# Kernel optimization log

Hardware: AMD Instinct MI355X
Metric: run time of the kernel (lower is better)

Reference implementation:

```python
import jax, jax.numpy as jnp
import numpy as np


def _scattering(image, mags, phases):
    # image: [B,S,S] real; mags/phases: [J,L,S,S] real (Fourier-domain Morlet filters)
    J = mags.shape[0]
    psi = (mags * jnp.exp(1j * phases)).astype(jnp.complex64)        # [J,L,S,S]
    xf = jnp.fft.fft2(image)                                          # [B,S,S] complex64
    # first-order: modulus of wavelet convolutions, all scales/orientations at once
    u1 = jnp.abs(jnp.fft.ifft2(xf[:, None, None] * psi[None]))        # [B,J,L,S,S]
    s0 = image.mean(axis=(-2, -1))                                    # [B]
    s1 = u1.mean(axis=(2, 3, 4))                                      # [B,J] (orientation-averaged)
    # second-order: only j2 > j1 (the nan-filtered entries in the original)
    s2_parts = []
    for j1 in range(J - 1):  # structural loop over scales, not data dims
        u1f = jnp.fft.fft2(u1[:, j1].astype(jnp.complex64))           # [B,L1,S,S]
        psi2 = psi[j1 + 1:]                                           # [J2,L2,S,S]
        v = jnp.abs(jnp.fft.ifft2(u1f[:, :, None, None] * psi2[None, None]))  # [B,L1,J2,L2,S,S]
        s2_parts.append(v.mean(axis=(1, 3, 4, 5)))                    # [B,J2]
    s2 = jnp.concatenate(s2_parts, axis=1)                            # [B, J*(J-1)/2]
    return s0, s1, s2


def setup_inputs() -> dict:
    key = jax.random.key(0)
    ks = jax.random.split(key, 8)
    B, S, J, L = 64, 128, 6, 4
    return {
        "image_batch": jax.random.normal(ks[0], (B, S, S), dtype=jnp.float32),
        "mags": jax.random.uniform(ks[1], (J, L, S, S), dtype=jnp.float32),
        "phases": jax.random.normal(ks[2], (J, L, S, S), dtype=jnp.float32),
        "w1": jax.random.normal(ks[3], (22, 16), dtype=jnp.float32) * 0.1,
        "b1": jnp.zeros((16,), dtype=jnp.float32),
        "w2": jax.random.normal(ks[4], (16, 16), dtype=jnp.float32) * 0.1,
        "b2": jnp.zeros((16,), dtype=jnp.float32),
        "w3": jax.random.normal(ks[5], (16, 1), dtype=jnp.float32) * 0.1,
        "b3": jnp.zeros((1,), dtype=jnp.float32),
    }


def reference(image_batch, mags, phases, w1, b1, w2, b2, w3, b3):
    s0, s1, s2 = _scattering(image_batch, mags, phases)
    x = jnp.concatenate([s0[:, None], s1, s2], axis=1)                # [B,22]
    x = jax.nn.relu(x @ w1 + b1)
    x = jax.nn.relu(x @ w2 + b2)
    x = jax.nn.sigmoid(x @ w3 + b3)
    return jnp.squeeze(x, axis=1)                                     # [B]
```

## Files before the change

kernel.cpp:

```cpp
#include <hip/hip_runtime.h>
#include <math.h>


#define SDIM 128
#define PLANE 16384
#define PITCH 129
#define NT 1024
#define TWO_PI 6.28318530717958647692f
#define PSIH_SCALE 16.0f
#define A_SCALE 16.0f

typedef _Float16 h2 __attribute__((ext_vector_type(2)));

constexpr float W16R[8] = {1.f, 0.9238795325f, 0.7071067812f, 0.3826834324f,
                           0.f, -0.3826834324f, -0.7071067812f, -0.9238795325f};
constexpr float W16I[8] = {0.f, -0.3826834324f, -0.7071067812f, -0.9238795325f,
                           -1.f, -0.9238795325f, -0.7071067812f, -0.3826834324f};

__device__ __forceinline__ float fast_sqrtf(float x) { return __builtin_amdgcn_sqrtf(x); }

__device__ __forceinline__ unsigned packbf(float re, float im) {
  const unsigned r = __float_as_uint(re) + 0x8000u;
  const unsigned i = __float_as_uint(im) + 0x8000u;
  return __builtin_amdgcn_perm(r, i, 0x07060302u);
}
__device__ __forceinline__ void unpackbf(unsigned u, float& re, float& im) {
  re = __uint_as_float(u & 0xFFFF0000u);
  im = __uint_as_float(u << 16);
}

union UHU { unsigned u; h2 h; };
__device__ __forceinline__ h2 u2h(unsigned u) { UHU x; x.u = u; return x.h; }
__device__ __forceinline__ unsigned h2u(h2 h) { UHU x; x.h = h; return x.u; }
__device__ __forceinline__ h2 bch2(float f) { const _Float16 h = (_Float16)f; h2 v = {h, h}; return v; }
__device__ __forceinline__ h2 mkh2(float a, float b) { h2 v = {(_Float16)a, (_Float16)b}; return v; }

#define SEL_LO 0x05040100u
#define SEL_HI 0x07060302u

__device__ __forceinline__ void stC(float2* s, int idx, float re, float im) { s[idx] = make_float2(re, im); }
__device__ __forceinline__ void ldC(const float2* s, int idx, float& re, float& im) { const float2 v = s[idx]; re = v.x; im = v.y; }
__device__ __forceinline__ void stC(unsigned* s, int idx, float re, float im) { s[idx] = packbf(re, im); }
__device__ __forceinline__ void ldC(const unsigned* s, int idx, float& re, float& im) { unpackbf(s[idx], re, im); }

__device__ __forceinline__ void load_tw(const float2* __restrict__ twg, int g,
                                        float* twr, float* twi) {
#pragma unroll
  for (int k = 1; k < 16; ++k) {
    const float2 w = twg[16 * g + k];
    twr[k] = __uint_as_float(__builtin_amdgcn_readfirstlane(__float_as_uint(w.x)));
    twi[k] = __uint_as_float(__builtin_amdgcn_readfirstlane(__float_as_uint(w.y)));
  }
}
__device__ __forceinline__ void load_twh(const uint2* __restrict__ twgh, int g,
                                         unsigned* twru, unsigned* twiu) {
#pragma unroll
  for (int k = 1; k < 16; ++k) {
    const uint2 w = twgh[16 * g + k];
    twru[k] = (unsigned)__builtin_amdgcn_readfirstlane((int)w.x);
    twiu[k] = (unsigned)__builtin_amdgcn_readfirstlane((int)w.y);
  }
}

template<bool INV>
__device__ __forceinline__ void bfly(float& ar, float& ai, float& br, float& bi, const int idx) {
  float tr, ti;
  if (idx == 0) { tr = br; ti = bi; }
  else if (idx == 4) {
    if (INV) { tr = -bi; ti = br; } else { tr = bi; ti = -br; }
  } else {
    const float wr = W16R[idx];
    const float wi = INV ? -W16I[idx] : W16I[idx];
    tr = br * wr - bi * wi;
    ti = br * wi + bi * wr;
  }
  br = ar - tr; bi = ai - ti;
  ar = ar + tr; ai = ai + ti;
}

#define CSWAP(re, im, a, b) { float _t = re[a]; re[a]=re[b]; re[b]=_t; _t = im[a]; im[a]=im[b]; im[b]=_t; }

template<bool INV>
__device__ __forceinline__ void dft16(float* re, float* im) {
  CSWAP(re, im, 1, 8) CSWAP(re, im, 2, 4) CSWAP(re, im, 3, 12)
  CSWAP(re, im, 5, 10) CSWAP(re, im, 7, 14) CSWAP(re, im, 11, 13)
#pragma unroll
  for (int ls = 1; ls <= 4; ++ls) {
    const int len = 1 << ls, half = len >> 1, tstep = 16 >> ls;
#pragma unroll
    for (int blk = 0; blk < 16; blk += len)
#pragma unroll
      for (int j = 0; j < half; ++j)
        bfly<INV>(re[blk + j], im[blk + j], re[blk + j + half], im[blk + j + half], j * tstep);
  }
}

template<bool INV>
__device__ __forceinline__ void dft8(float* re, float* im) {
  CSWAP(re, im, 1, 4) CSWAP(re, im, 3, 6)
#pragma unroll
  for (int ls = 1; ls <= 3; ++ls) {
    const int len = 1 << ls, half = len >> 1, tstep = 8 >> ls;
#pragma unroll
    for (int blk = 0; blk < 8; blk += len)
#pragma unroll
      for (int j = 0; j < half; ++j)
        bfly<INV>(re[blk + j], im[blk + j], re[blk + j + half], im[blk + j + half], j * tstep * 2);
  }
}

__device__ __forceinline__ void twmul_fwd(float* R, float* I, const float* twr, const float* twi) {
#pragma unroll
  for (int k = 1; k < 16; ++k) {
    const float r = R[k] * twr[k] - I[k] * twi[k];
    I[k] = R[k] * twi[k] + I[k] * twr[k]; R[k] = r;
  }
}
__device__ __forceinline__ void twmul_inv(float* R, float* I, const float* twr, const float* twi) {
#pragma unroll
  for (int k = 1; k < 16; ++k) {
    const float r = R[k] * twr[k] + I[k] * twi[k];
    I[k] = I[k] * twr[k] - R[k] * twi[k]; R[k] = r;
  }
}

template<typename S>
__device__ __forceinline__ void fwd_fft2(float* R, float* I, S* sC,
                                         int g, int q, const float* twr, const float* twi) {
  const int rb = q * PITCH;
  dft16<false>(R, I);
  twmul_fwd(R, I, twr, twi);
  __syncthreads();
#pragma unroll
  for (int k = 0; k < 16; ++k) stC(sC, rb + 8 * k + g, R[k], I[k]);
  __syncthreads();
#pragma unroll
  for (int t = 0; t < 8; ++t) {
    ldC(sC, rb + 16 * g + t, R[t], I[t]);
    ldC(sC, rb + 16 * g + 8 + t, R[8 + t], I[8 + t]);
  }
  dft8<false>(R, I); dft8<false>(R + 8, I + 8);
#pragma unroll
  for (int k2 = 0; k2 < 8; ++k2) {
    stC(sC, rb + 16 * g + k2, R[k2], I[k2]);
    stC(sC, rb + 16 * g + 8 + k2, R[8 + k2], I[8 + k2]);
  }
  __syncthreads();
#pragma unroll
  for (int m = 0; m < 16; ++m) ldC(sC, (g + 8 * m) * PITCH + q, R[m], I[m]);
  dft16<false>(R, I);
  twmul_fwd(R, I, twr, twi);
#pragma unroll
  for (int k = 0; k < 16; ++k) stC(sC, (8 * k + g) * PITCH + q, R[k], I[k]);
  __syncthreads();
#pragma unroll
  for (int u = 0; u < 8; ++u) {
    const int bp = (16 * g + 2 * u) * PITCH + q;
    ldC(sC, bp, R[2 * u], I[2 * u]);
    ldC(sC, bp + PITCH, R[2 * u + 1], I[2 * u + 1]);
  }
  dft8<false>(R, I); dft8<false>(R + 8, I + 8);
}

template<bool FIRST, typename S>
__device__ __forceinline__ void inv_fft2(float* R, float* I, S* sC,
                                         int g, int q, const float* twr, const float* twi) {
  const int rb = q * PITCH;
  dft8<true>(R, I); dft8<true>(R + 8, I + 8);
  if constexpr (!FIRST) __syncthreads();
#pragma unroll
  for (int t = 0; t < 16; ++t) stC(sC, rb + 16 * g + t, R[t], I[t]);
  __syncthreads();
#pragma unroll
  for (int k = 0; k < 16; ++k) ldC(sC, rb + 8 * k + g, R[k], I[k]);
  twmul_inv(R, I, twr, twi);
  dft16<true>(R, I);
#pragma unroll
  for (int m = 0; m < 16; ++m) stC(sC, rb + g + 8 * m, R[m], I[m]);
  __syncthreads();
#pragma unroll
  for (int u = 0; u < 8; ++u) {
    const int bp = (16 * g + 2 * u) * PITCH + q;
    ldC(sC, bp, R[2 * u], I[2 * u]);
    ldC(sC, bp + PITCH, R[2 * u + 1], I[2 * u + 1]);
  }
  dft8<true>(R, I); dft8<true>(R + 8, I + 8);
#pragma unroll
  for (int u = 0; u < 8; ++u) {
    const int bp = (16 * g + 2 * u) * PITCH + q;
    stC(sC, bp, R[2 * u], I[2 * u]);
    stC(sC, bp + PITCH, R[2 * u + 1], I[2 * u + 1]);
  }
  __syncthreads();
#pragma unroll
  for (int k = 0; k < 16; ++k) ldC(sC, (8 * k + g) * PITCH + q, R[k], I[k]);
  twmul_inv(R, I, twr, twi);
  dft16<true>(R, I);
}

template<bool INV>
__device__ __forceinline__ void bfly_h(h2& ar, h2& ai, h2& br, h2& bi, const int idx) {
  h2 tr, ti;
  if (idx == 0) { tr = br; ti = bi; }
  else if (idx == 4) {
    if (INV) { tr = -bi; ti = br; } else { tr = bi; ti = -br; }
  } else {
    const h2 wr = bch2(W16R[idx]);
    const h2 wi = bch2(INV ? -W16I[idx] : W16I[idx]);
    tr = br * wr - bi * wi;
    ti = br * wi + bi * wr;
  }
  br = ar - tr; bi = ai - ti;
  ar = ar + tr; ai = ai + ti;
}

#define HSWAP(re, im, a, b) { h2 _t = re[a]; re[a]=re[b]; re[b]=_t; _t = im[a]; im[a]=im[b]; im[b]=_t; }

template<bool INV>
__device__ __forceinline__ void dft16h(h2* re, h2* im) {
  HSWAP(re, im, 1, 8) HSWAP(re, im, 2, 4) HSWAP(re, im, 3, 12)
  HSWAP(re, im, 5, 10) HSWAP(re, im, 7, 14) HSWAP(re, im, 11, 13)
#pragma unroll
  for (int ls = 1; ls <= 4; ++ls) {
    const int len = 1 << ls, half = len >> 1, tstep = 16 >> ls;
#pragma unroll
    for (int blk = 0; blk < 16; blk += len)
#pragma unroll
      for (int j = 0; j < half; ++j)
        bfly_h<INV>(re[blk + j], im[blk + j], re[blk + j + half], im[blk + j + half], j * tstep);
  }
}

template<bool INV>
__device__ __forceinline__ void dft8h(h2* re, h2* im) {
  HSWAP(re, im, 1, 4) HSWAP(re, im, 3, 6)
#pragma unroll
  for (int ls = 1; ls <= 3; ++ls) {
    const int len = 1 << ls, half = len >> 1, tstep = 8 >> ls;
#pragma unroll
    for (int blk = 0; blk < 8; blk += len)
#pragma unroll
      for (int j = 0; j < half; ++j)
        bfly_h<INV>(re[blk + j], im[blk + j], re[blk + j + half], im[blk + j + half], j * tstep * 2);
  }
}

__device__ __forceinline__ void twmul_inv_h(h2* R, h2* I, const unsigned* twru, const unsigned* twiu) {
#pragma unroll
  for (int k = 1; k < 16; ++k) {
    const h2 wr = u2h(twru[k]), wi = u2h(twiu[k]);
    const h2 r = R[k] * wr + I[k] * wi;
    I[k] = I[k] * wr - R[k] * wi;
    R[k] = r;
  }
}
__device__ __forceinline__ void twmul_fwd_h(h2* R, h2* I, const unsigned* twru, const unsigned* twiu) {
#pragma unroll
  for (int k = 1; k < 16; ++k) {
    const h2 wr = u2h(twru[k]), wi = u2h(twiu[k]);
    const h2 r = R[k] * wr - I[k] * wi;
    I[k] = R[k] * wi + I[k] * wr;
    R[k] = r;
  }
}

__device__ __forceinline__ void inv_rp_core(h2* R2, h2* I2, uint2* sU,
                                            int g, int q,
                                            const unsigned* twru, const unsigned* twiu) {
  const int sb = q * PITCH;
  dft8h<true>(R2, I2); dft8h<true>(R2 + 8, I2 + 8);
#pragma unroll
  for (int s = 0; s < 16; ++s) sU[sb + 16 * g + s] = make_uint2(h2u(R2[s]), h2u(I2[s]));
  __syncthreads();
#pragma unroll
  for (int k = 0; k < 16; ++k) { const uint2 v = sU[sb + 8 * k + g]; R2[k] = u2h(v.x); I2[k] = u2h(v.y); }
  twmul_inv_h(R2, I2, twru, twiu);
  dft16h<true>(R2, I2);
#pragma unroll
  for (int m = 0; m < 16; ++m) sU[sb + g + 8 * m] = make_uint2(h2u(R2[m]), h2u(I2[m]));
  __syncthreads();
  {
    const int s_base = (16 * g) & 63;
    const unsigned sel = (g < 4) ? SEL_LO : SEL_HI;
#pragma unroll
    for (int j = 0; j < 16; ++j) {
      const int cb = (s_base + j) * PITCH;
      const uint2 vA = sU[cb + q];
      const uint2 vB = sU[cb + q + 64];
      R2[j] = u2h(__builtin_amdgcn_perm(vB.x, vA.x, sel));
      I2[j] = u2h(__builtin_amdgcn_perm(vB.y, vA.y, sel));
    }
  }
  dft8h<true>(R2, I2); dft8h<true>(R2 + 8, I2 + 8);
  __syncthreads();
#pragma unroll
  for (int s = 0; s < 16; ++s) sU[sb + 16 * g + s] = make_uint2(h2u(R2[s]), h2u(I2[s]));
  __syncthreads();
#pragma unroll
  for (int k = 0; k < 16; ++k) { const uint2 v = sU[sb + 8 * k + g]; R2[k] = u2h(v.x); I2[k] = u2h(v.y); }
  twmul_inv_h(R2, I2, twru, twiu);
  dft16h<true>(R2, I2);
}

__device__ __forceinline__ void fwd_rp_core(h2* R2, h2* I2, uint2* sU,
                                            int g, int q,
                                            const unsigned* twru, const unsigned* twiu) {
  const int sb = q * PITCH;
  dft16h<false>(R2, I2);
  twmul_fwd_h(R2, I2, twru, twiu);
#pragma unroll
  for (int k = 0; k < 16; ++k) sU[sb + 8 * k + g] = make_uint2(h2u(R2[k]), h2u(I2[k]));
  __syncthreads();
#pragma unroll
  for (int t = 0; t < 16; ++t) { const uint2 v = sU[sb + 16 * g + t]; R2[t] = u2h(v.x); I2[t] = u2h(v.y); }
  dft8h<false>(R2, I2); dft8h<false>(R2 + 8, I2 + 8);
#pragma unroll
  for (int t = 0; t < 16; ++t) sU[sb + 16 * g + t] = make_uint2(h2u(R2[t]), h2u(I2[t]));
  __syncthreads();
  {
#pragma unroll
    for (int u = 0; u < 8; ++u) {
      const int cb = (g + 8 * u) * PITCH;
      const uint2 vA = sU[cb + q];
      const uint2 vB = sU[cb + q + 64];
      R2[u]     = u2h(__builtin_amdgcn_perm(vB.x, vA.x, SEL_LO));
      I2[u]     = u2h(__builtin_amdgcn_perm(vB.y, vA.y, SEL_LO));
      R2[u + 8] = u2h(__builtin_amdgcn_perm(vB.x, vA.x, SEL_HI));
      I2[u + 8] = u2h(__builtin_amdgcn_perm(vB.y, vA.y, SEL_HI));
    }
  }
  dft16h<false>(R2, I2);
  twmul_fwd_h(R2, I2, twru, twiu);
  __syncthreads();
#pragma unroll
  for (int k = 0; k < 16; ++k) sU[sb + 8 * k + g] = make_uint2(h2u(R2[k]), h2u(I2[k]));
  __syncthreads();
#pragma unroll
  for (int t = 0; t < 16; ++t) { const uint2 v = sU[sb + 16 * g + t]; R2[t] = u2h(v.x); I2[t] = u2h(v.y); }
  dft8h<false>(R2, I2); dft8h<false>(R2 + 8, I2 + 8);
}

template<int NW>
__device__ __forceinline__ float block_reduce_sum(float v, float* red, int tid) {
#pragma unroll
  for (int o = 32; o > 0; o >>= 1) v += __shfl_down(v, o);
  __syncthreads();
  if ((tid & 63) == 0) red[tid >> 6] = v;
  __syncthreads();
  float t = 0.0f;
  if (tid == 0) {
#pragma unroll
    for (int w = 0; w < NW; ++w) t += red[w];
  }
  return t;
}

__global__ __launch_bounds__(256) void k_psi(const float* __restrict__ mags,
                                             const float* __restrict__ phases,
                                             float2* __restrict__ psi,
                                             float2* __restrict__ twg,
                                             uint2* __restrict__ psih,
                                             uint2* __restrict__ twgh) {
  if (blockIdx.x == 0 && threadIdx.x < 128) {
    const int gg = threadIdx.x >> 4, k = threadIdx.x & 15;
    float sn, cs;
    __sincosf(-TWO_PI * (float)(gg * k) * (1.0f / 128.0f), &sn, &cs);
    twg[threadIdx.x] = make_float2(cs, sn);
    twgh[threadIdx.x] = make_uint2(h2u(bch2(cs)), h2u(bch2(sn)));
  }
  const int gid = blockIdx.x * 256 + threadIdx.x;
  if (gid < 24 * PLANE) {
    const int p = gid >> 14;
    const int rem = gid & (PLANE - 1);
    const int e = rem & 1;
    const int tt = (rem >> 1) & 1023;
    const int i = rem >> 11;
    const int j = 2 * i + e;
    const int g = tt >> 7, q = tt & 127;
    const int pr = 16 * g + j, pc = q;
    const int kr = (pr >> 3) + 16 * (pr & 7);
    const int kc = (pc >> 3) + 16 * (pc & 7);
    const int src = (p << 14) + kr * SDIM + kc;
    const float m = mags[src] * (1.0f / 16384.0f);
    float sn, cs;
    __sincosf(phases[src], &sn, &cs);
    psi[gid] = make_float2(m * cs, m * sn);
  } else if (gid < 24 * PLANE + 20 * 8192) {
    const int c = gid - 24 * PLANE;
    const int pidx = c >> 13;
    const int rem = c & 8191;
    const int j = rem >> 9;
    const int t512 = rem & 511;
    const int g = t512 >> 6, q = t512 & 63;
    const int row = 16 * g + j;
    const int plane = pidx + 4;
    const int kr = (row >> 3) + 16 * (row & 7);
    const int kc0 = (q >> 3) + 16 * (q & 7);
    const int q1 = q + 64;
    const int kc1 = (q1 >> 3) + 16 * (q1 & 7);
    const int src0 = (plane << 14) + kr * SDIM + kc0;
    const int src1 = (plane << 14) + kr * SDIM + kc1;
    const float scl = PSIH_SCALE / 16384.0f;
    const float m0 = mags[src0] * scl;
    const float m1 = mags[src1] * scl;
    float sn0, cs0, sn1, cs1;
    __sincosf(phases[src0], &sn0, &cs0);
    __sincosf(phases[src1], &sn1, &cs1);
    psih[c] = make_uint2(h2u(mkh2(m0 * cs0, m1 * cs1)), h2u(mkh2(m0 * sn0, m1 * sn1)));
  }
}

__global__ __launch_bounds__(NT) void k_img_fft(const float* __restrict__ img,
                                                float2* __restrict__ Xf,
                                                float* __restrict__ s0,
                                                const float2* __restrict__ twg) {
  __shared__ float2 sC[SDIM * PITCH];
  __shared__ float red[16];
  const int tid = threadIdx.x, b = blockIdx.x;
  const int g = __builtin_amdgcn_readfirstlane(tid >> 7);
  const int q = tid & 127;
  float twr[16], twi[16];
  load_tw(twg, g, twr, twi);
  const float* ip = img + b * PLANE;
  float sum = 0.0f;
#pragma unroll
  for (int kk = 0; kk < 16; ++kk) {
    const int e = tid + kk * NT;
    const float v = ip[e];
    sC[(e >> 7) * PITCH + (e & 127)] = make_float2(v, 0.0f);
    sum += v;
  }
  const float tot = block_reduce_sum<16>(sum, red, tid);
  if (tid == 0) s0[b] = tot * (1.0f / 16384.0f);
  __syncthreads();
  float R[16], I[16];
#pragma unroll
  for (int m = 0; m < 16; ++m) { R[m] = sC[q * PITCH + g + 8 * m].x; I[m] = 0.0f; }
  fwd_fft2(R, I, sC, g, q, twr, twi);
  float4* x4 = (float4*)Xf + (size_t)b * 8192 + tid;
#pragma unroll
  for (int i = 0; i < 8; ++i)
    x4[i * 1024] = make_float4(R[2 * i], I[2 * i], R[2 * i + 1], I[2 * i + 1]);
}

__global__ __launch_bounds__(512, 4) void k_scat_a_rp(const float2* __restrict__ Xf,
                                                      const float2* __restrict__ psi,
                                                      float* __restrict__ s1num,
                                                      unsigned* __restrict__ Ubuf,
                                                      const uint2* __restrict__ twgh) {
  __shared__ uint2 sU[64 * PITCH];
  __shared__ float red[8];
  const int tid = threadIdx.x;
  const int g = __builtin_amdgcn_readfirstlane(tid >> 6);
  const int q = tid & 63;
  unsigned twru[16], twiu[16];
  load_twh(twgh, g, twru, twiu);
  const int bid = blockIdx.x;

  int plane, b, sidx, grp = -1;
  if (bid < 1280) {
    const int j1 = bid >> 8;
    b = (bid & 255) >> 2;
    const int l1 = bid & 3;
    plane = j1 * 4 + l1;
    sidx = b * 6 + j1;
    grp = (b * 5 + j1) * 4 + l1;
  } else {
    const int idx = bid - 1280;
    b = idx >> 2;
    plane = 20 + (idx & 3);
    sidx = b * 6 + 5;
  }

  h2 R2[16], I2[16];
  {
    const int t0 = g * 128 + q;
    const float4* xL = (const float4*)Xf + (size_t)b * 8192 + t0;
    const float4* pL = (const float4*)psi + (size_t)plane * 8192 + t0;
#pragma unroll
    for (int i = 0; i < 8; ++i) {
      const float4 xa = xL[i * 1024],      va = pL[i * 1024];
      const float4 xb = xL[i * 1024 + 64], vb = pL[i * 1024 + 64];
      const float reL0 = xa.x * va.x - xa.y * va.y, imL0 = xa.x * va.y + xa.y * va.x;
      const float reH0 = xb.x * vb.x - xb.y * vb.y, imH0 = xb.x * vb.y + xb.y * vb.x;
      const float reL1 = xa.z * va.z - xa.w * va.w, imL1 = xa.z * va.w + xa.w * va.z;
      const float reH1 = xb.z * vb.z - xb.w * vb.w, imH1 = xb.z * vb.w + xb.w * vb.z;
      R2[2 * i]     = mkh2(reL0 * A_SCALE, reH0 * A_SCALE);
      I2[2 * i]     = mkh2(imL0 * A_SCALE, imH0 * A_SCALE);
      R2[2 * i + 1] = mkh2(reL1 * A_SCALE, reH1 * A_SCALE);
      I2[2 * i + 1] = mkh2(imL1 * A_SCALE, imH1 * A_SCALE);
    }
  }
  inv_rp_core(R2, I2, sU, g, q, twru, twiu);

  float s1sum = 0.0f;
  if (grp >= 0) {
#pragma unroll
    for (int m = 0; m < 16; ++m) {
      const float rl = (float)R2[m].x, il = (float)I2[m].x;
      const float rh = (float)R2[m].y, ih = (float)I2[m].y;
      const float aL = fast_sqrtf(rl * rl + il * il);
      const float aH = fast_sqrtf(rh * rh + ih * ih);
      s1sum += aL + aH;
      R2[m] = mkh2(aL * (1.0f / A_SCALE), aH * (1.0f / A_SCALE));
      I2[m] = bch2(0.0f);
    }
    fwd_rp_core(R2, I2, sU, g, q, twru, twiu);
    uint4* o4 = (uint4*)Ubuf + (size_t)grp * 4096 + tid;
#pragma unroll
    for (int i = 0; i < 8; ++i) {
      uint4 ob;
      ob.x = __builtin_amdgcn_perm(h2u(I2[2 * i]),     h2u(R2[2 * i]),     SEL_LO);
      ob.y = __builtin_amdgcn_perm(h2u(I2[2 * i]),     h2u(R2[2 * i]),     SEL_HI);
      ob.z = __builtin_amdgcn_perm(h2u(I2[2 * i + 1]), h2u(R2[2 * i + 1]), SEL_LO);
      ob.w = __builtin_amdgcn_perm(h2u(I2[2 * i + 1]), h2u(R2[2 * i + 1]), SEL_HI);
      o4[i * 512] = ob;
    }
  } else {
#pragma unroll
    for (int m = 0; m < 16; ++m) {
      const float rl = (float)R2[m].x, il = (float)I2[m].x;
      const float rh = (float)R2[m].y, ih = (float)I2[m].y;
      s1sum += fast_sqrtf(rl * rl + il * il) + fast_sqrtf(rh * rh + ih * ih);
    }
  }
  const float tot = block_reduce_sum<8>(s1sum, red, tid);
  if (tid == 0) atomicAdd(&s1num[sidx], tot);
}

__global__ __launch_bounds__(NT) void k_scat_a(const float2* __restrict__ Xf,
                                               const float2* __restrict__ psi,
                                               float* __restrict__ s1num,
                                               unsigned* __restrict__ Ubuf,
                                               const float2* __restrict__ twg) {
  __shared__ unsigned sU[SDIM * PITCH];
  __shared__ float red[16];
  const int tid = threadIdx.x;
  const int g = __builtin_amdgcn_readfirstlane(tid >> 7);
  const int q = tid & 127;
  float twr[16], twi[16];
  load_tw(twg, g, twr, twi);
  const int bid = blockIdx.x;
  float R[16], I[16];

  if (bid < 1280) {
    const int j1 = bid >> 8;
    const int b = (bid & 255) >> 2;
    const int l1 = bid & 3;
    const float4* x4 = (const float4*)Xf + (size_t)b * 8192 + tid;
    const float4* p4 = (const float4*)psi + (size_t)(j1 * 4 + l1) * 8192 + tid;
#pragma unroll
    for (int i = 0; i < 8; ++i) {
      const float4 x = x4[i * 1024], v = p4[i * 1024];
      R[2 * i]     = x.x * v.x - x.y * v.y;  I[2 * i]     = x.x * v.y + x.y * v.x;
      R[2 * i + 1] = x.z * v.z - x.w * v.w;  I[2 * i + 1] = x.z * v.w + x.w * v.z;
    }
    inv_fft2<true>(R, I, sU, g, q, twr, twi);
    float s1sum = 0.0f;
#pragma unroll
    for (int m = 0; m < 16; ++m) {
      const float a = fast_sqrtf(R[m] * R[m] + I[m] * I[m]);
      s1sum += a; R[m] = a; I[m] = 0.0f;
    }
    fwd_fft2(R, I, sU, g, q, twr, twi);
    uint4 ob[4];
    unsigned* obs = (unsigned*)ob;
#pragma unroll
    for (int j = 0; j < 16; ++j) obs[j] = packbf(R[j], I[j]);
    uint4* o4 = (uint4*)Ubuf + (size_t)((b * 5 + j1) * 4 + l1) * 4096 + tid;
#pragma unroll
    for (int i = 0; i < 4; ++i) o4[i * 1024] = ob[i];
    const float tot = block_reduce_sum<16>(s1sum, red, tid);
    if (tid == 0) atomicAdd(&s1num[b * 6 + j1], tot);
  } else {
    const int idx = bid - 1280;
    const int b = idx >> 2, l = idx & 3;
    const float4* x4 = (const float4*)Xf + (size_t)b * 8192 + tid;
    const float4* p4 = (const float4*)psi + (size_t)(20 + l) * 8192 + tid;
#pragma unroll
    for (int i = 0; i < 8; ++i) {
      const float4 x = x4[i * 1024], v = p4[i * 1024];
      R[2 * i]     = x.x * v.x - x.y * v.y;  I[2 * i]     = x.x * v.y + x.y * v.x;
      R[2 * i + 1] = x.z * v.z - x.w * v.w;  I[2 * i + 1] = x.z * v.w + x.w * v.z;
    }
    inv_fft2<true>(R, I, sU, g, q, twr, twi);
    float s = 0.0f;
#pragma unroll
    for (int m = 0; m < 16; ++m) s += fast_sqrtf(R[m] * R[m] + I[m] * I[m]);
    const float tot = block_reduce_sum<16>(s, red, tid);
    if (tid == 0) atomicAdd(&s1num[b * 6 + 5], tot);
  }
}

__global__ __launch_bounds__(512, 4) void k_scat_b_rpm(const uint2* __restrict__ psih,
                                                       const unsigned* __restrict__ Ubuf,
                                                       float* __restrict__ s2num,
                                                       const uint2* __restrict__ twgh) {
  __shared__ uint2 sU[64 * PITCH];
  __shared__ float red[8];
  const int tid = threadIdx.x;
  const int g = __builtin_amdgcn_readfirstlane(tid >> 6);
  const int q = tid & 63;
  unsigned twru[16], twiu[16];
  load_twh(twgh, g, twru, twiu);
  const int bid = blockIdx.x;
  const int j1 = bid >> 8;
  const int b = (bid & 255) >> 2;
  const int l1 = bid & 3;
  const int pb = (j1 * (11 - j1)) >> 1;
  const int nit = (5 - j1) * 4;

  h2 UR2[16], UI2[16];
  {
    const uint4* u4 = (const uint4*)Ubuf + (size_t)((b * 5 + j1) * 4 + l1) * 4096 + tid;
#pragma unroll
    for (int i = 0; i < 8; ++i) {
      const uint4 v = u4[i * 512];
      UR2[2 * i]     = u2h(__builtin_amdgcn_perm(v.y, v.x, SEL_LO));
      UI2[2 * i]     = u2h(__builtin_amdgcn_perm(v.y, v.x, SEL_HI));
      UR2[2 * i + 1] = u2h(__builtin_amdgcn_perm(v.w, v.z, SEL_LO));
      UI2[2 * i + 1] = u2h(__builtin_amdgcn_perm(v.w, v.z, SEL_HI));
    }
  }

  uint2 buf[16];
  {
    const uint2* ph = psih + (size_t)(4 * j1) * 8192 + tid;
#pragma unroll
    for (int j = 0; j < 16; ++j) buf[j] = ph[j * 512];
  }

  float vsum = 0.0f;
  for (int it = 0; it < nit; ++it) {
    h2 R2[16], I2[16];
#pragma unroll
    for (int j = 0; j < 16; ++j) {
      const h2 pr = u2h(buf[j].x), pi = u2h(buf[j].y);
      R2[j] = UR2[j] * pr - UI2[j] * pi;
      I2[j] = UR2[j] * pi + UI2[j] * pr;
    }
    if (it + 1 < nit) {
      const uint2* phn = psih + (size_t)(4 * j1 + it + 1) * 8192 + tid;
#pragma unroll
      for (int j = 0; j < 16; ++j) buf[j] = phn[j * 512];
    }
    if (it) __syncthreads();
    inv_rp_core(R2, I2, sU, g, q, twru, twiu);
#pragma unroll
    for (int m = 0; m < 16; ++m) {
      const float rl = (float)R2[m].x, il = (float)I2[m].x;
      const float rh = (float)R2[m].y, ih = (float)I2[m].y;
      vsum += fast_sqrtf(rl * rl + il * il) + fast_sqrtf(rh * rh + ih * ih);
    }
    if ((it & 3) == 3) {
      const float tot = block_reduce_sum<8>(vsum, red, tid);
      if (tid == 0) atomicAdd(&s2num[b * 15 + pb + (it >> 2)], tot);
      vsum = 0.0f;
    }
  }
}

__global__ __launch_bounds__(NT) void k_scat_b(const float2* __restrict__ psi,
                                               const unsigned* __restrict__ Ubuf,
                                               float* __restrict__ s2num,
                                               const float2* __restrict__ twg) {
  __shared__ unsigned sU[SDIM * PITCH];
  __shared__ float red[16];
  const int tid = threadIdx.x;
  const int g = __builtin_amdgcn_readfirstlane(tid >> 7);
  const int q = tid & 127;
  float twr[16], twi[16];
  load_tw(twg, g, twr, twi);
  int t = blockIdx.x;
  const int l2 = t & 3; t >>= 2;
  const int pair = t % 15; t /= 15;
  const int l1 = t & 3;
  const int b = t >> 2;
  int j1 = 0, base = 0;
  if (pair >= 14)      { j1 = 4; base = 14; }
  else if (pair >= 12) { j1 = 3; base = 12; }
  else if (pair >= 9)  { j1 = 2; base = 9; }
  else if (pair >= 5)  { j1 = 1; base = 5; }
  const int j2 = j1 + 1 + (pair - base);
  float R[16], I[16];
  {
    const uint4* u4 = (const uint4*)Ubuf + (size_t)((b * 5 + j1) * 4 + l1) * 4096 + tid;
    uint4 ub[4];
#pragma unroll
    for (int i = 0; i < 4; ++i) ub[i] = u4[i * 1024];
    const unsigned* ubs = (const unsigned*)ub;
    const float4* p4 = (const float4*)psi + (size_t)(j2 * 4 + l2) * 8192 + tid;
#pragma unroll
    for (int i = 0; i < 8; ++i) {
      const float4 v = p4[i * 1024];
      float ur, ui;
      unpackbf(ubs[2 * i], ur, ui);
      R[2 * i] = ur * v.x - ui * v.y;      I[2 * i] = ur * v.y + ui * v.x;
      unpackbf(ubs[2 * i + 1], ur, ui);
      R[2 * i + 1] = ur * v.z - ui * v.w;  I[2 * i + 1] = ur * v.w + ui * v.z;
    }
  }
  inv_fft2<true>(R, I, sU, g, q, twr, twi);
  float vsum = 0.0f;
#pragma unroll
  for (int m = 0; m < 16; ++m) vsum += fast_sqrtf(R[m] * R[m] + I[m] * I[m]);
  const float tot = block_reduce_sum<16>(vsum, red, tid);
  if (tid == 0) atomicAdd(&s2num[b * 15 + pair], tot);
}

__global__ __launch_bounds__(NT) void k_scat_mono(const float2* __restrict__ Xf,
                                                  const float2* __restrict__ psi,
                                                  float* __restrict__ s1num,
                                                  float* __restrict__ s2num,
                                                  const float2* __restrict__ twg) {
  __shared__ unsigned sU[SDIM * PITCH];
  __shared__ float red[16];
  const int tid = threadIdx.x;
  const int g = __builtin_amdgcn_readfirstlane(tid >> 7);
  const int q = tid & 127;
  float twr[16], twi[16];
  load_tw(twg, g, twr, twi);
  const int bid = blockIdx.x;
  float R[16], I[16];
  if (bid < 1280) {
    const int j1 = bid >> 8;
    const int b = (bid & 255) >> 2;
    const int l1 = bid & 3;
    const float4* x4 = (const float4*)Xf + (size_t)b * 8192 + tid;
    const float4* p4 = (const float4*)psi + (size_t)(j1 * 4 + l1) * 8192 + tid;
#pragma unroll
    for (int i = 0; i < 8; ++i) {
      const float4 x = x4[i * 1024], v = p4[i * 1024];
      R[2 * i]     = x.x * v.x - x.y * v.y;  I[2 * i]     = x.x * v.y + x.y * v.x;
      R[2 * i + 1] = x.z * v.z - x.w * v.w;  I[2 * i + 1] = x.z * v.w + x.w * v.z;
    }
    inv_fft2<true>(R, I, sU, g, q, twr, twi);
    float s1sum = 0.0f;
#pragma unroll
    for (int m = 0; m < 16; ++m) {
      const float a = fast_sqrtf(R[m] * R[m] + I[m] * I[m]);
      s1sum += a; R[m] = a; I[m] = 0.0f;
    }
    fwd_fft2(R, I, sU, g, q, twr, twi);
    float Ur[16], Ui[16];
#pragma unroll
    for (int k = 0; k < 16; ++k) { Ur[k] = R[k]; Ui[k] = I[k]; }
    {
      const float tot = block_reduce_sum<16>(s1sum, red, tid);
      if (tid == 0) atomicAdd(&s1num[b * 6 + j1], tot);
    }
    const int pb = (j1 * (11 - j1)) >> 1;
    int plane = (j1 + 1) * 4;
#pragma unroll 1
    for (int j2 = j1 + 1; j2 <= 5; ++j2) {
      float vsum = 0.0f;
#pragma unroll 1
      for (int l2 = 0; l2 < 4; ++l2) {
        const float4* q4 = (const float4*)psi + (size_t)plane * 8192 + tid;
#pragma unroll
        for (int i = 0; i < 8; ++i) {
          const float4 v = q4[i * 1024];
          R[2 * i]     = Ur[2 * i] * v.x - Ui[2 * i] * v.y;
          I[2 * i]     = Ur[2 * i] * v.y + Ui[2 * i] * v.x;
          R[2 * i + 1] = Ur[2 * i + 1] * v.z - Ui[2 * i + 1] * v.w;
          I[2 * i + 1] = Ur[2 * i + 1] * v.w + Ui[2 * i + 1] * v.z;
        }
        inv_fft2<false>(R, I, sU, g, q, twr, twi);
#pragma unroll
        for (int m = 0; m < 16; ++m) vsum += fast_sqrtf(R[m] * R[m] + I[m] * I[m]);
        ++plane;
      }
      const float tot = block_reduce_sum<16>(vsum, red, tid);
      if (tid == 0) atomicAdd(&s2num[b * 15 + pb + (j2 - j1 - 1)], tot);
    }
  } else {
    const int idx = bid - 1280;
    const int b = idx >> 2, l = idx & 3;
    const float4* x4 = (const float4*)Xf + (size_t)b * 8192 + tid;
    const float4* p4 = (const float4*)psi + (size_t)(20 + l) * 8192 + tid;
#pragma unroll
    for (int i = 0; i < 8; ++i) {
      const float4 x = x4[i * 1024], v = p4[i * 1024];
      R[2 * i]     = x.x * v.x - x.y * v.y;  I[2 * i]     = x.x * v.y + x.y * v.x;
      R[2 * i + 1] = x.z * v.z - x.w * v.w;  I[2 * i + 1] = x.z * v.w + x.w * v.z;
    }
    inv_fft2<true>(R, I, sU, g, q, twr, twi);
    float s = 0.0f;
#pragma unroll
    for (int m = 0; m < 16; ++m) s += fast_sqrtf(R[m] * R[m] + I[m] * I[m]);
    const float tot = block_reduce_sum<16>(s, red, tid);
    if (tid == 0) atomicAdd(&s1num[b * 6 + 5], tot);
  }
}

__global__ __launch_bounds__(64) void k_final(const float* __restrict__ s0,
                                              const float* __restrict__ s1num,
                                              const float* __restrict__ s2num,
                                              const float* __restrict__ w1,
                                              const float* __restrict__ b1,
                                              const float* __restrict__ w2,
                                              const float* __restrict__ b2,
                                              const float* __restrict__ w3,
                                              const float* __restrict__ b3,
                                              float* __restrict__ out,
                                              float s1scale, float s2scale) {
  const int b = threadIdx.x;
  if (b >= 64) return;
  float x[22];
  x[0] = s0[b];
#pragma unroll
  for (int j = 0; j < 6; ++j) x[1 + j] = s1num[b * 6 + j] * s1scale;
#pragma unroll
  for (int p = 0; p < 15; ++p) x[7 + p] = s2num[b * 15 + p] * s2scale;
  float h1[16];
#pragma unroll
  for (int o = 0; o < 16; ++o) {
    float t = b1[o];
    for (int i = 0; i < 22; ++i) t += x[i] * w1[i * 16 + o];
    h1[o] = fmaxf(t, 0.0f);
  }
  float h2a[16];
#pragma unroll
  for (int o = 0; o < 16; ++o) {
    float t = b2[o];
    for (int i = 0; i < 16; ++i) t += h1[i] * w2[i * 16 + o];
    h2a[o] = fmaxf(t, 0.0f);
  }
  float t = b3[0];
#pragma unroll
  for (int i = 0; i < 16; ++i) t += h2a[i] * w3[i];
  out[b] = 1.0f / (1.0f + expf(-t));
}

extern "C" void kernel_launch(void* const* d_in, const int* in_sizes, int n_in,
                              void* d_out, int out_size, void* d_ws, size_t ws_size,
                              hipStream_t stream) {
  (void)in_sizes; (void)n_in; (void)out_size;
  const float* image  = (const float*)d_in[0];
  const float* mags   = (const float*)d_in[1];
  const float* phases = (const float*)d_in[2];
  const float* w1 = (const float*)d_in[3];
  const float* b1 = (const float*)d_in[4];
  const float* w2 = (const float*)d_in[5];
  const float* b2 = (const float*)d_in[6];
  const float* w3 = (const float*)d_in[7];
  const float* b3 = (const float*)d_in[8];
  float* out = (float*)d_out;

  char* ws = (char*)d_ws;
  float2* psi = (float2*)ws;
  float2* Xf  = (float2*)(ws + 3145728);
  float*  s0  = (float*)(ws + 11534336);
  float*  s1n = s0 + 64;
  float*  s2n = s1n + 384;
  float2* twg = (float2*)(s2n + 960);
  uint2*  twgh = (uint2*)((char*)twg + 1024);
  unsigned* Ubuf = (unsigned*)(ws + 11542528);
  uint2*  psih = (uint2*)(ws + 95428608);
  const size_t need_r5 = 11542528ull + 83886080ull;
  const size_t need_h2 = need_r5 + 1310720ull;

  hipMemsetAsync(s1n, 0, (384 + 960) * sizeof(float), stream);
  if (ws_size >= need_h2) {
    k_psi<<<dim3(2176), dim3(256), 0, stream>>>(mags, phases, psi, twg, psih, twgh);
    k_img_fft<<<dim3(64), dim3(NT), 0, stream>>>(image, Xf, s0, twg);
    k_scat_a_rp<<<dim3(1536), dim3(512), 0, stream>>>(Xf, psi, s1n, Ubuf, twgh);
    k_scat_b_rpm<<<dim3(1280), dim3(512), 0, stream>>>(psih, Ubuf, s2n, twgh);
    k_final<<<dim3(1), dim3(64), 0, stream>>>(s0, s1n, s2n, w1, b1, w2, b2, w3, b3, out,
                                              1.0f / (4.0f * 16384.0f * A_SCALE),
                                              1.0f / (16.0f * 16384.0f * PSIH_SCALE));
  } else if (ws_size >= need_r5) {
    k_psi<<<dim3(1536), dim3(256), 0, stream>>>(mags, phases, psi, twg, psih, twgh);
    k_img_fft<<<dim3(64), dim3(NT), 0, stream>>>(image, Xf, s0, twg);
    k_scat_a<<<dim3(1536), dim3(NT), 0, stream>>>(Xf, psi, s1n, Ubuf, twg);
    k_scat_b<<<dim3(15360), dim3(NT), 0, stream>>>(psi, Ubuf, s2n, twg);
    k_final<<<dim3(1), dim3(64), 0, stream>>>(s0, s1n, s2n, w1, b1, w2, b2, w3, b3, out,
                                              1.0f / (4.0f * 16384.0f),
                                              1.0f / (16.0f * 16384.0f));
  } else {
    k_psi<<<dim3(1536), dim3(256), 0, stream>>>(mags, phases, psi, twg, psih, twgh);
    k_img_fft<<<dim3(64), dim3(NT), 0, stream>>>(image, Xf, s0, twg);
    k_scat_mono<<<dim3(1536), dim3(NT), 0, stream>>>(Xf, psi, s1n, s2n, twg);
    k_final<<<dim3(1), dim3(64), 0, stream>>>(s0, s1n, s2n, w1, b1, w2, b2, w3, b3, out,
                                              1.0f / (4.0f * 16384.0f),
                                              1.0f / (16.0f * 16384.0f));
  }
}
```

Before: 440.7 us.

## Fuse first- and second-order scattering kernels to keep U1 spectra in registers

Merges the first-order kernel and the second-order kernel into one kernel. Each block now keeps its forward-transformed modulus spectrum in registers and loops directly over the j2/l2 filters, instead of writing the fp16 spectra to a global buffer and reading them back. The modulus computations also move to packed half-precision squaring before the sqrt. This drops a launch and a large global round trip, but gives uneven per-block work (j1=0 blocks do 20 iterations, j1=4 blocks only 4), raises register pressure, and squaring in fp16 risks overflow or precision loss.

```diff
diff --git a/kernel.cpp b/kernel.cpp
--- a/kernel.cpp
+++ b/kernel.cpp
@@ -443,11 +443,12 @@
     x4[i * 1024] = make_float4(R[2 * i], I[2 * i], R[2 * i + 1], I[2 * i + 1]);
 }
 
-__global__ __launch_bounds__(512, 4) void k_scat_a_rp(const float2* __restrict__ Xf,
-                                                      const float2* __restrict__ psi,
-                                                      float* __restrict__ s1num,
-                                                      unsigned* __restrict__ Ubuf,
-                                                      const uint2* __restrict__ twgh) {
+__global__ __launch_bounds__(512, 4) void k_scat_ab(const float2* __restrict__ Xf,
+                                                    const float2* __restrict__ psi,
+                                                    const uint2* __restrict__ psih,
+                                                    float* __restrict__ s1num,
+                                                    float* __restrict__ s2num,
+                                                    const uint2* __restrict__ twgh) {
   __shared__ uint2 sU[64 * PITCH];
   __shared__ float red[8];
   const int tid = threadIdx.x;
@@ -457,14 +458,13 @@
   load_twh(twgh, g, twru, twiu);
   const int bid = blockIdx.x;
 
-  int plane, b, sidx, grp = -1;
+  int plane, b, sidx, j1 = -1;
   if (bid < 1280) {
-    const int j1 = bid >> 8;
+    j1 = bid >> 8;
     b = (bid & 255) >> 2;
     const int l1 = bid & 3;
     plane = j1 * 4 + l1;
     sidx = b * 6 + j1;
-    grp = (b * 5 + j1) * 4 + l1;
   } else {
     const int idx = bid - 1280;
     b = idx >> 2;
@@ -493,39 +493,72 @@
   }
   inv_rp_core(R2, I2, sU, g, q, twru, twiu);
 
+  if (j1 < 0) {
+    float s1sum = 0.0f;
+#pragma unroll
+    for (int m = 0; m < 16; ++m) {
+      const h2 sq = R2[m] * R2[m] + I2[m] * I2[m];
+      s1sum += fast_sqrtf((float)sq.x) + fast_sqrtf((float)sq.y);
+    }
+    const float tot = block_reduce_sum<8>(s1sum, red, tid);
+    if (tid == 0) atomicAdd(&s1num[sidx], tot);
+    return;
+  }
+
   float s1sum = 0.0f;
-  if (grp >= 0) {
+#pragma unroll
+  for (int m = 0; m < 16; ++m) {
+    const h2 sq = R2[m] * R2[m] + I2[m] * I2[m];
+    const float aL = fast_sqrtf((float)sq.x);
+    const float aH = fast_sqrtf((float)sq.y);
+    s1sum += aL + aH;
+    R2[m] = mkh2(aL * (1.0f / A_SCALE), aH * (1.0f / A_SCALE));
+    I2[m] = bch2(0.0f);
+  }
+  fwd_rp_core(R2, I2, sU, g, q, twru, twiu);
+
+  h2 UR2[16], UI2[16];
+#pragma unroll
+  for (int j = 0; j < 16; ++j) { UR2[j] = R2[j]; UI2[j] = I2[j]; }
+  uint2 buf[16];
+  {
+    const uint2* ph = psih + (size_t)(4 * j1) * 8192 + tid;
+#pragma unroll
+    for (int j = 0; j < 16; ++j) buf[j] = ph[j * 512];
+  }
+  {
+    const float tot = block_reduce_sum<8>(s1sum, red, tid);
+    if (tid == 0) atomicAdd(&s1num[sidx], tot);
+  }
+
+  const int pb = (j1 * (11 - j1)) >> 1;
+  const int nit = (5 - j1) * 4;
+  float vsum = 0.0f;
+  for (int it = 0; it < nit; ++it) {
+#pragma unroll
+    for (int j = 0; j < 16; ++j) {
+      const h2 pr = u2h(buf[j].x), pi = u2h(buf[j].y);
+      R2[j] = UR2[j] * pr - UI2[j] * pi;
+      I2[j] = UR2[j] * pi + UI2[j] * pr;
+    }
+    if (it + 1 < nit) {
+      const uint2* phn = psih + (size_t)(4 * j1 + it + 1) * 8192 + tid;
+#pragma unroll
+      for (int j = 0; j < 16; ++j) buf[j] = phn[j * 512];
+    }
+    __syncthreads();
+    inv_rp_core(R2, I2, sU, g, q, twru, twiu);
 #pragma unroll
     for (int m = 0; m < 16; ++m) {
-      const float rl = (float)R2[m].x, il = (float)I2[m].x;
-      const float rh = (float)R2[m].y, ih = (float)I2[m].y;
-      const float aL = fast_sqrtf(rl * rl + il * il);
-      const float aH = fast_sqrtf(rh * rh + ih * ih);
-      s1sum += aL + aH;
-      R2[m] = mkh2(aL * (1.0f / A_SCALE), aH * (1.0f / A_SCALE));
-      I2[m] = bch2(0.0f);
-    }
-    fwd_rp_core(R2, I2, sU, g, q, twru, twiu);
-    uint4* o4 = (uint4*)Ubuf + (size_t)grp * 4096 + tid;
-#pragma unroll
-    for (int i = 0; i < 8; ++i) {
-      uint4 ob;
-      ob.x = __builtin_amdgcn_perm(h2u(I2[2 * i]),     h2u(R2[2 * i]),     SEL_LO);
-      ob.y = __builtin_amdgcn_perm(h2u(I2[2 * i]),     h2u(R2[2 * i]),     SEL_HI);
-      ob.z = __builtin_amdgcn_perm(h2u(I2[2 * i + 1]), h2u(R2[2 * i + 1]), SEL_LO);
-      ob.w = __builtin_amdgcn_perm(h2u(I2[2 * i + 1]), h2u(R2[2 * i + 1]), SEL_HI);
-      o4[i * 512] = ob;
-    }
-  } else {
-#pragma unroll
-    for (int m = 0; m < 16; ++m) {
-      const float rl = (float)R2[m].x, il = (float)I2[m].x;
-      const float rh = (float)R2[m].y, ih = (float)I2[m].y;
-      s1sum += fast_sqrtf(rl * rl + il * il) + fast_sqrtf(rh * rh + ih * ih);
-    }
-  }
-  const float tot = block_reduce_sum<8>(s1sum, red, tid);
-  if (tid == 0) atomicAdd(&s1num[sidx], tot);
+      const h2 sq = R2[m] * R2[m] + I2[m] * I2[m];
+      vsum += fast_sqrtf((float)sq.x) + fast_sqrtf((float)sq.y);
+    }
+    if ((it & 3) == 3) {
+      const float tot = block_reduce_sum<8>(vsum, red, tid);
+      if (tid == 0) atomicAdd(&s2num[b * 15 + pb + (it >> 2)], tot);
+      vsum = 0.0f;
+    }
+  }
 }
 
 __global__ __launch_bounds__(NT) void k_scat_a(const float2* __restrict__ Xf,
@@ -589,74 +622,6 @@
     for (int m = 0; m < 16; ++m) s += fast_sqrtf(R[m] * R[m] + I[m] * I[m]);
     const float tot = block_reduce_sum<16>(s, red, tid);
     if (tid == 0) atomicAdd(&s1num[b * 6 + 5], tot);
-  }
-}
-
-__global__ __launch_bounds__(512, 4) void k_scat_b_rpm(const uint2* __restrict__ psih,
-                                                       const unsigned* __restrict__ Ubuf,
-                                                       float* __restrict__ s2num,
-                                                       const uint2* __restrict__ twgh) {
-  __shared__ uint2 sU[64 * PITCH];
-  __shared__ float red[8];
-  const int tid = threadIdx.x;
-  const int g = __builtin_amdgcn_readfirstlane(tid >> 6);
-  const int q = tid & 63;
-  unsigned twru[16], twiu[16];
-  load_twh(twgh, g, twru, twiu);
-  const int bid = blockIdx.x;
-  const int j1 = bid >> 8;
-  const int b = (bid & 255) >> 2;
-  const int l1 = bid & 3;
-  const int pb = (j1 * (11 - j1)) >> 1;
-  const int nit = (5 - j1) * 4;
-
-  h2 UR2[16], UI2[16];
-  {
-    const uint4* u4 = (const uint4*)Ubuf + (size_t)((b * 5 + j1) * 4 + l1) * 4096 + tid;
-#pragma unroll
-    for (int i = 0; i < 8; ++i) {
-      const uint4 v = u4[i * 512];
-      UR2[2 * i]     = u2h(__builtin_amdgcn_perm(v.y, v.x, SEL_LO));
-      UI2[2 * i]     = u2h(__builtin_amdgcn_perm(v.y, v.x, SEL_HI));
-      UR2[2 * i + 1] = u2h(__builtin_amdgcn_perm(v.w, v.z, SEL_LO));
-      UI2[2 * i + 1] = u2h(__builtin_amdgcn_perm(v.w, v.z, SEL_HI));
-    }
-  }
-
-  uint2 buf[16];
-  {
-    const uint2* ph = psih + (size_t)(4 * j1) * 8192 + tid;
-#pragma unroll
-    for (int j = 0; j < 16; ++j) buf[j] = ph[j * 512];
-  }
-
-  float vsum = 0.0f;
-  for (int it = 0; it < nit; ++it) {
-    h2 R2[16], I2[16];
-#pragma unroll
-    for (int j = 0; j < 16; ++j) {
-      const h2 pr = u2h(buf[j].x), pi = u2h(buf[j].y);
-      R2[j] = UR2[j] * pr - UI2[j] * pi;
-      I2[j] = UR2[j] * pi + UI2[j] * pr;
-    }
-    if (it + 1 < nit) {
-      const uint2* phn = psih + (size_t)(4 * j1 + it + 1) * 8192 + tid;
-#pragma unroll
-      for (int j = 0; j < 16; ++j) buf[j] = phn[j * 512];
-    }
-    if (it) __syncthreads();
-    inv_rp_core(R2, I2, sU, g, q, twru, twiu);
-#pragma unroll
-    for (int m = 0; m < 16; ++m) {
-      const float rl = (float)R2[m].x, il = (float)I2[m].x;
-      const float rh = (float)R2[m].y, ih = (float)I2[m].y;
-      vsum += fast_sqrtf(rl * rl + il * il) + fast_sqrtf(rh * rh + ih * ih);
-    }
-    if ((it & 3) == 3) {
-      const float tot = block_reduce_sum<8>(vsum, red, tid);
-      if (tid == 0) atomicAdd(&s2num[b * 15 + pb + (it >> 2)], tot);
-      vsum = 0.0f;
-    }
   }
 }
 
@@ -864,8 +829,7 @@
   if (ws_size >= need_h2) {
     k_psi<<<dim3(2176), dim3(256), 0, stream>>>(mags, phases, psi, twg, psih, twgh);
     k_img_fft<<<dim3(64), dim3(NT), 0, stream>>>(image, Xf, s0, twg);
-    k_scat_a_rp<<<dim3(1536), dim3(512), 0, stream>>>(Xf, psi, s1n, Ubuf, twgh);
-    k_scat_b_rpm<<<dim3(1280), dim3(512), 0, stream>>>(psih, Ubuf, s2n, twgh);
+    k_scat_ab<<<dim3(1536), dim3(512), 0, stream>>>(Xf, psi, psih, s1n, s2n, twgh);
     k_final<<<dim3(1), dim3(64), 0, stream>>>(s0, s1n, s2n, w1, b1, w2, b2, w3, b3, out,
                                               1.0f / (4.0f * 16384.0f * A_SCALE),
                                               1.0f / (16.0f * 16384.0f * PSIH_SCALE));
```

Result: faster. 424.8 us (-3.6%).
